# Kernel tuning notes

Hardware: AMD Instinct MI355X
Metric: run time of the kernel (lower is better)

## Reference

```python
import jax, jax.numpy as jnp
import numpy as np

N_QUBITS = 12
N_QLAYERS = 2
BATCH = 1024
DIM = 2 ** N_QUBITS


def _apply_1q(state, U, wire):
    # state: (B, 2**n) complex; U: (2,2) shared or (B,2,2) batched
    B = state.shape[0]
    s = state.reshape(B, 2 ** wire, 2, -1)
    if U.ndim == 2:
        s = jnp.einsum('ij,bajc->baic', U, s)
    else:
        s = jnp.einsum('bij,bajc->baic', U, s)
    return s.reshape(B, DIM)


def _apply_cnot(state, c, t):
    # CNOT with control c, target t on flat state (B, 2**n)
    B = state.shape[0]
    a, b = min(c, t), max(c, t)
    s = state.reshape(B, 2 ** a, 2, 2 ** (b - a - 1), 2, -1)
    ctrl_ax, tgt_ax = (2, 4) if c < t else (4, 2)
    s0 = jnp.take(s, 0, axis=ctrl_ax)
    s1 = jnp.take(s, 1, axis=ctrl_ax)
    flip_ax = tgt_ax - 1 if tgt_ax > ctrl_ax else tgt_ax
    s1 = jnp.flip(s1, axis=flip_ax)  # X on target where control==1
    return jnp.stack([s0, s1], axis=ctrl_ax).reshape(B, DIM)


def _ry_batched(theta):
    # theta: (B,) -> (B,2,2) RY(theta) matrices
    c = jnp.cos(theta * 0.5)
    s = jnp.sin(theta * 0.5)
    U = jnp.stack([jnp.stack([c, -s], -1), jnp.stack([s, c], -1)], -2)
    return U.astype(jnp.complex64)


def _rot(phi, theta, omega):
    # PennyLane Rot = RZ(omega) @ RY(theta) @ RZ(phi)
    c = jnp.cos(theta * 0.5)
    s = jnp.sin(theta * 0.5)
    em = jnp.exp(-0.5j * (phi + omega))   # e^{-i(phi+omega)/2}
    ep = jnp.exp(0.5j * (phi + omega))
    ed = jnp.exp(0.5j * (phi - omega))    # e^{ i(phi-omega)/2}
    edm = jnp.exp(-0.5j * (phi - omega))
    row0 = jnp.stack([em * c, -ed * s])
    row1 = jnp.stack([edm * s, ep * c])
    return jnp.stack([row0, row1]).astype(jnp.complex64)


def _circuit(x, weights):
    B = x.shape[0]
    state = jnp.zeros((B, DIM), jnp.complex64).at[:, 0].set(1.0)
    for l in range(N_QLAYERS):
        # AngleEmbedding: RY(x[:, q]) on each wire (data re-uploading)
        for q in range(N_QUBITS):
            state = _apply_1q(state, _ry_batched(x[:, q]), q)
        # StronglyEntanglingLayers (single layer slice): Rot per wire
        for q in range(N_QUBITS):
            w = weights[l, q]
            state = _apply_1q(state, _rot(w[0], w[1], w[2]), q)
        # range-1 CNOT ring (single-layer SEL => r = 1)
        for q in range(N_QUBITS):
            state = _apply_cnot(state, q, (q + 1) % N_QUBITS)
    probs = state.real ** 2 + state.imag ** 2  # (B, 2**n)
    outs = []
    for q in range(N_QUBITS):
        p = probs.reshape(B, 2 ** q, 2, -1)
        outs.append(jnp.sum(p[:, :, 0, :], axis=(1, 2)) - jnp.sum(p[:, :, 1, :], axis=(1, 2)))
    return jnp.stack(outs, axis=1)  # (B, n_qubits) <Z_q> expvals


def setup_inputs() -> dict:
    key = jax.random.key(0)
    k1, k2 = jax.random.split(key)
    x = jax.random.uniform(k1, (BATCH, N_QUBITS), jnp.float32, 0.0, 2.0 * np.pi)
    weights = jax.random.normal(k2, (N_QLAYERS, N_QUBITS, 3), jnp.float32)
    return {"x": x, "weights": weights}


def reference(x, weights):
    return _circuit(x, weights)
```

## Files before the change

kernel.cpp:

```cpp
#include <hip/hip_runtime.h>

#define NQ 12
#define NT 64
#define EPB 4


struct cpx { float x, y; };
__device__ __forceinline__ cpx cmul(cpx a, cpx b) {
    return { a.x * b.x - a.y * b.y, a.x * b.y + a.y * b.x };
}
__device__ __forceinline__ cpx cmulc(cpx a, cpx b) {
    return { a.x * b.x + a.y * b.y, a.y * b.x - a.x * b.y };
}
__device__ __forceinline__ cpx cadd(cpx a, cpx b) { return { a.x + b.x, a.y + b.y }; }
__device__ __forceinline__ cpx csub(cpx a, cpx b) { return { a.x - b.x, a.y - b.y }; }
__device__ __forceinline__ cpx shflc(cpx a, int lane) {
    cpx r; r.x = __shfl(a.x, lane, 64); r.y = __shfl(a.y, lane, 64); return r;
}

__global__ __launch_bounds__(NT) void qsim_kernel(
    const float* __restrict__ x,
    const float* __restrict__ w,
    float* __restrict__ out)
{
    __shared__ float fm[EPB][2][NQ][8];
    __shared__ cpx Amat[EPB][9][16], Bmat[EPB][9][16];
    __shared__ cpx gS[EPB][4][4];
    __shared__ cpx h0U[EPB][4], h0S[EPB][4], h11U[EPB][4], h11S[EPB][4];
    __shared__ cpx Rv[EPB][3][4][4];
    __shared__ cpx PBc[EPB][11][16];
    __shared__ cpx SAc[EPB][12][16];
    __shared__ float sval[EPB][48];

    const int t    = threadIdx.x;
    const int g    = t >> 4;
    const int u    = t & 15;
    const int base = t & 48;
    const int b0   = blockIdx.x * EPB;

    for (int task = t; task < EPB * 2 * NQ; task += NT) {
        int e = task / (2 * NQ);
        int rem = task % (2 * NQ);
        int l = rem / NQ, q = rem % NQ;
        float hy = 0.5f * x[(b0 + e) * NQ + q];
        float cy = cosf(hy), sy = sinf(hy);
        const float* wp = w + (l * NQ + q) * 3;
        float phi = wp[0], the = wp[1], om = wp[2];
        float c = cosf(0.5f * the), s = sinf(0.5f * the);
        float al = 0.5f * (phi + om), be = 0.5f * (phi - om);
        float ca = cosf(al), sa = sinf(al), cb = cosf(be), sb = sinf(be);
        float r00r =  ca * c, r00i = -sa * c;
        float r01r = -cb * s, r01i = -sb * s;
        float r10r =  cb * s, r10i = -sb * s;
        float r11r =  ca * c, r11i =  sa * c;
        float* m = fm[e][l][q];
        m[0] =  r00r * cy + r01r * sy;  m[1] =  r00i * cy + r01i * sy;
        m[2] = -r00r * sy + r01r * cy;  m[3] = -r00i * sy + r01i * cy;
        m[4] =  r10r * cy + r11r * sy;  m[5] =  r10i * cy + r11i * sy;
        m[6] = -r10r * sy + r11r * cy;  m[7] = -r10i * sy + r11i * cy;
    }
    __syncthreads();

    auto Vq = [&](int q, int bit) -> cpx {
        const float* m = &fm[g][0][q][bit ? 4 : 0]; return { m[0], m[1] };
    };
    auto Uq = [&](int q, int d, int c) -> cpx {
        const float* m = &fm[g][1][q][4 * d + 2 * c]; return { m[0], m[1] };
    };

    {
        const int a = (u >> 3) & 1, ap = (u >> 2) & 1, c = (u >> 1) & 1, cp = u & 1;
        for (int q = 2; q <= 10; ++q) {
            cpx t0 = cmul(Vq(q, c ^ a),  Uq(q, 0, c));
            cpx t1 = cmul(Vq(q, c ^ a),  Uq(q, 1, c));
            cpx p0 = cmul(Vq(q, cp ^ ap), Uq(q, 0, cp));
            cpx p1 = cmul(Vq(q, cp ^ ap), Uq(q, 1, cp));
            cpx e0 = cmulc(t0, p0), e1 = cmulc(t1, p1);
            Amat[g][q - 2][u] = cadd(e0, e1);
            Bmat[g][q - 2][u] = csub(e0, e1);
        }
        const int s = a, sp = ap, cc = c, ccp = cp;
        cpx l0 = cmul(Uq(1, 0, cc),  Vq(1, cc ^ s));
        cpx l1 = cmul(Uq(1, 1, cc),  Vq(1, cc ^ s));
        cpx m0 = cmul(Uq(1, 0, ccp), Vq(1, ccp ^ sp));
        cpx m1 = cmul(Uq(1, 1, ccp), Vq(1, ccp ^ sp));
        cpx gg = csub(cmulc(l0, m0), cmulc(l1, m1));
        cpx lw = cmulc(Vq(0, s), Vq(0, sp));
        gS[g][2 * s + sp][2 * cc + ccp] = cmul(gg, lw);
    }
    if (u < 4) {
        const int c0 = u >> 1, c0p = u & 1;
        cpx a0 = cmulc(Uq(0, 0, c0),  Uq(0, 0, c0p));
        cpx a1 = cmulc(Uq(0, 1, c0),  Uq(0, 1, c0p));
        h0U[g][u] = cadd(a0, a1);  h0S[g][u] = csub(a0, a1);
        cpx b0v = cmulc(Uq(11, 0, c0),  Uq(11, 0, c0p));
        cpx b1v = cmulc(Uq(11, 1, c0),  Uq(11, 1, c0p));
        h11U[g][u] = cadd(b0v, b1v);  h11S[g][u] = csub(b0v, b1v);
    }
    __syncthreads();

    {
        const int s = (u >> 3) & 1, sp = (u >> 2) & 1, c10 = (u >> 1) & 1, c10p = u & 1;
        for (int V = 0; V < 3; ++V) {
            const cpx* h0  = (V == 1) ? h0U[g]  : h0S[g];
            const cpx* h11 = (V == 0) ? h11U[g] : h11S[g];
            cpx acc = { 0.f, 0.f };
            for (int c0 = 0; c0 < 2; ++c0)
                for (int c0p = 0; c0p < 2; ++c0p) {
                    cpx term = cmul(h0[2 * c0 + c0p], h11[2 * (c0 ^ s) + (c0p ^ sp)]);
                    term = cmul(term, Vq(11, c0 ^ s ^ c10));
                    term = cmulc(term, Vq(11, c0p ^ sp ^ c10p));
                    acc = cadd(acc, term);
                }
            Rv[g][V][2 * s + sp][2 * c10 + c10p] = acc;
        }
    }
    __syncthreads();

    {
        const int R = u >> 2, C = u & 3;
        cpx cur = { (R == C) ? 1.f : 0.f, 0.f };
        PBc[g][1][u] = cur;
        for (int k = 2; k <= 10; ++k) {
            cpx nv = { 0.f, 0.f };
            for (int K = 0; K < 4; ++K)
                nv = cadd(nv, cmul(shflc(cur, base + 4 * R + K), Bmat[g][k - 2][4 * K + C]));
            cur = nv;
            PBc[g][k][u] = cur;
        }
        cur = { (R == C) ? 1.f : 0.f, 0.f };
        SAc[g][11][u] = cur;
        for (int k = 10; k >= 2; --k) {
            cpx nv = { 0.f, 0.f };
            for (int K = 0; K < 4; ++K)
                nv = cadd(nv, cmul(Amat[g][k - 2][4 * R + K], shflc(cur, base + 4 * K + C)));
            cur = nv;
            SAc[g][k][u] = cur;
        }
    }
    __syncthreads();

    for (int pi = u; pi < 48; pi += 16) {
        const int qq = pi >> 2, ssi = pi & 3;
        const int kk = (qq == 0 || qq == 11) ? 10 : qq;
        const int V  = (qq == 0) ? 1 : ((qq == 11) ? 2 : 0);
        cpx rowL[4], colR[4];
        for (int K = 0; K < 4; ++K) {
            cpx acc = { 0.f, 0.f };
            for (int R = 0; R < 4; ++R)
                acc = cadd(acc, cmul(gS[g][ssi][R], PBc[g][kk][4 * R + K]));
            rowL[K] = acc;
            cpx acc2 = { 0.f, 0.f };
            for (int C = 0; C < 4; ++C)
                acc2 = cadd(acc2, cmul(SAc[g][kk + 1][4 * K + C], Rv[g][V][ssi][C]));
            colR[K] = acc2;
        }
        cpx val = { 0.f, 0.f };
        for (int K = 0; K < 4; ++K) val = cadd(val, cmul(rowL[K], colR[K]));
        sval[g][pi] = val.x;
    }
    __syncthreads();

    if (t < EPB * NQ) {
        int e = t / NQ, q = t % NQ;
        out[(b0 + e) * NQ + q] =
            sval[e][4 * q] + sval[e][4 * q + 1] + sval[e][4 * q + 2] + sval[e][4 * q + 3];
    }
}

extern "C" void kernel_launch(void* const* d_in, const int* in_sizes, int n_in,
                              void* d_out, int out_size, void* d_ws, size_t ws_size,
                              hipStream_t stream) {
    int xi = 0, wi = 1;
    if (n_in >= 2 && in_sizes[1] > in_sizes[0]) { xi = 1; wi = 0; }
    const float* x = (const float*)d_in[xi];
    const float* w = (const float*)d_in[wi];
    float* out = (float*)d_out;
    const int B = in_sizes[xi] / NQ;
    qsim_kernel<<<B / EPB, NT, 0, stream>>>(x, w, out);
}
```

Baseline: 60.20 us.

## Process one batch element per block and split per-element stages across thread groups

Each block now handles a single batch element with 64 threads instead of four elements with 16 threads each. Within a block the gate-matrix construction, the forward and backward transfer-matrix chains, and the boundary terms are spread across the thread groups so they run concurrently. One barrier is removed, and the final reduction uses wave shuffles instead of shared memory. Trig calls switch to fast intrinsics, which may reduce accuracy. The grid grows fourfold, and several phases leave many lanes idle.

Measured after the change: 58.08 us. 3.5% less time.

```diff
diff --git a/kernel.cpp b/kernel.cpp
--- a/kernel.cpp
+++ b/kernel.cpp
@@ -2,7 +2,6 @@
 
 #define NQ 12
 #define NT 64
-#define EPB 4
 
 
 struct cpx { float x, y; };
@@ -23,37 +22,34 @@
     const float* __restrict__ w,
     float* __restrict__ out)
 {
-    __shared__ float fm[EPB][2][NQ][8];
-    __shared__ cpx Amat[EPB][9][16], Bmat[EPB][9][16];
-    __shared__ cpx gS[EPB][4][4];
-    __shared__ cpx h0U[EPB][4], h0S[EPB][4], h11U[EPB][4], h11S[EPB][4];
-    __shared__ cpx Rv[EPB][3][4][4];
-    __shared__ cpx PBc[EPB][11][16];
-    __shared__ cpx SAc[EPB][12][16];
-    __shared__ float sval[EPB][48];
+    __shared__ float fm[2][NQ][8];
+    __shared__ cpx Amat[9][16], Bmat[9][16];
+    __shared__ cpx gS[4][4];
+    __shared__ cpx h0U[4], h0S[4], h11U[4], h11S[4];
+    __shared__ cpx Rv[3][4][4];
+    __shared__ cpx PBc[11][16];
+    __shared__ cpx SAc[12][16];
 
-    const int t    = threadIdx.x;
-    const int g    = t >> 4;
-    const int u    = t & 15;
-    const int base = t & 48;
-    const int b0   = blockIdx.x * EPB;
+    const int t   = threadIdx.x;
+    const int u   = t & 15;
+    const int grp = t >> 4;
+    const int b   = blockIdx.x;
 
-    for (int task = t; task < EPB * 2 * NQ; task += NT) {
-        int e = task / (2 * NQ);
-        int rem = task % (2 * NQ);
-        int l = rem / NQ, q = rem % NQ;
-        float hy = 0.5f * x[(b0 + e) * NQ + q];
-        float cy = cosf(hy), sy = sinf(hy);
+    if (t < 2 * NQ) {
+        const int l = (t >= NQ) ? 1 : 0;
+        const int q = t - l * NQ;
+        float hy = 0.5f * x[b * NQ + q];
+        float cy = __cosf(hy), sy = __sinf(hy);
         const float* wp = w + (l * NQ + q) * 3;
         float phi = wp[0], the = wp[1], om = wp[2];
-        float c = cosf(0.5f * the), s = sinf(0.5f * the);
+        float cth = __cosf(0.5f * the), sth = __sinf(0.5f * the);
         float al = 0.5f * (phi + om), be = 0.5f * (phi - om);
-        float ca = cosf(al), sa = sinf(al), cb = cosf(be), sb = sinf(be);
-        float r00r =  ca * c, r00i = -sa * c;
-        float r01r = -cb * s, r01i = -sb * s;
-        float r10r =  cb * s, r10i = -sb * s;
-        float r11r =  ca * c, r11i =  sa * c;
-        float* m = fm[e][l][q];
+        float ca = __cosf(al), sa = __sinf(al), cb = __cosf(be), sb = __sinf(be);
+        float r00r =  ca * cth, r00i = -sa * cth;
+        float r01r = -cb * sth, r01i = -sb * sth;
+        float r10r =  cb * sth, r10i = -sb * sth;
+        float r11r =  ca * cth, r11i =  sa * cth;
+        float* m = fm[l][q];
         m[0] =  r00r * cy + r01r * sy;  m[1] =  r00i * cy + r01i * sy;
         m[2] = -r00r * sy + r01r * cy;  m[3] = -r00i * sy + r01i * cy;
         m[4] =  r10r * cy + r11r * sy;  m[5] =  r10i * cy + r11i * sy;
@@ -62,23 +58,26 @@
     __syncthreads();
 
     auto Vq = [&](int q, int bit) -> cpx {
-        const float* m = &fm[g][0][q][bit ? 4 : 0]; return { m[0], m[1] };
+        const float* m = &fm[0][q][bit ? 4 : 0]; return { m[0], m[1] };
     };
     auto Uq = [&](int q, int d, int c) -> cpx {
-        const float* m = &fm[g][1][q][4 * d + 2 * c]; return { m[0], m[1] };
+        const float* m = &fm[1][q][4 * d + 2 * c]; return { m[0], m[1] };
     };
 
-    {
-        const int a = (u >> 3) & 1, ap = (u >> 2) & 1, c = (u >> 1) & 1, cp = u & 1;
-        for (int q = 2; q <= 10; ++q) {
+    const int a = (u >> 3) & 1, ap = (u >> 2) & 1, c = (u >> 1) & 1, cp = u & 1;
+    if (grp < 3) {
+        #pragma unroll
+        for (int r = 0; r < 3; ++r) {
+            const int q = 2 + 3 * grp + r;
             cpx t0 = cmul(Vq(q, c ^ a),  Uq(q, 0, c));
             cpx t1 = cmul(Vq(q, c ^ a),  Uq(q, 1, c));
             cpx p0 = cmul(Vq(q, cp ^ ap), Uq(q, 0, cp));
             cpx p1 = cmul(Vq(q, cp ^ ap), Uq(q, 1, cp));
             cpx e0 = cmulc(t0, p0), e1 = cmulc(t1, p1);
-            Amat[g][q - 2][u] = cadd(e0, e1);
-            Bmat[g][q - 2][u] = csub(e0, e1);
+            Amat[q - 2][u] = cadd(e0, e1);
+            Bmat[q - 2][u] = csub(e0, e1);
         }
+    } else {
         const int s = a, sp = ap, cc = c, ccp = cp;
         cpx l0 = cmul(Uq(1, 0, cc),  Vq(1, cc ^ s));
         cpx l1 = cmul(Uq(1, 1, cc),  Vq(1, cc ^ s));
@@ -86,85 +85,88 @@
         cpx m1 = cmul(Uq(1, 1, ccp), Vq(1, ccp ^ sp));
         cpx gg = csub(cmulc(l0, m0), cmulc(l1, m1));
         cpx lw = cmulc(Vq(0, s), Vq(0, sp));
-        gS[g][2 * s + sp][2 * cc + ccp] = cmul(gg, lw);
-    }
-    if (u < 4) {
-        const int c0 = u >> 1, c0p = u & 1;
-        cpx a0 = cmulc(Uq(0, 0, c0),  Uq(0, 0, c0p));
-        cpx a1 = cmulc(Uq(0, 1, c0),  Uq(0, 1, c0p));
-        h0U[g][u] = cadd(a0, a1);  h0S[g][u] = csub(a0, a1);
-        cpx b0v = cmulc(Uq(11, 0, c0),  Uq(11, 0, c0p));
-        cpx b1v = cmulc(Uq(11, 1, c0),  Uq(11, 1, c0p));
-        h11U[g][u] = cadd(b0v, b1v);  h11S[g][u] = csub(b0v, b1v);
+        gS[2 * s + sp][2 * cc + ccp] = cmul(gg, lw);
+        if (u < 4) {
+            const int c0 = u >> 1, c0p = u & 1;
+            cpx a0 = cmulc(Uq(0, 0, c0),  Uq(0, 0, c0p));
+            cpx a1 = cmulc(Uq(0, 1, c0),  Uq(0, 1, c0p));
+            h0U[u] = cadd(a0, a1);  h0S[u] = csub(a0, a1);
+            cpx b0v = cmulc(Uq(11, 0, c0),  Uq(11, 0, c0p));
+            cpx b1v = cmulc(Uq(11, 1, c0),  Uq(11, 1, c0p));
+            h11U[u] = cadd(b0v, b1v);  h11S[u] = csub(b0v, b1v);
+        }
     }
     __syncthreads();
 
-    {
-        const int s = (u >> 3) & 1, sp = (u >> 2) & 1, c10 = (u >> 1) & 1, c10p = u & 1;
-        for (int V = 0; V < 3; ++V) {
-            const cpx* h0  = (V == 1) ? h0U[g]  : h0S[g];
-            const cpx* h11 = (V == 0) ? h11U[g] : h11S[g];
+    if (t < 32) {
+        const int R = u >> 2, C = u & 3;
+        const bool isA = (t >= 16);
+        const int base = t & 48;
+        cpx rhs[9][4];
+        #pragma unroll
+        for (int i = 0; i < 9; ++i)
+            #pragma unroll
+            for (int K = 0; K < 4; ++K)
+                rhs[i][K] = isA ? Amat[8 - i][4 * C + K] : Bmat[i][4 * K + C];
+        cpx cur = { (R == C) ? 1.f : 0.f, 0.f };
+        { cpx* dst = isA ? &SAc[11][4 * C + R] : &PBc[1][u]; *dst = cur; }
+        #pragma unroll
+        for (int i = 0; i < 9; ++i) {
+            cpx nv = { 0.f, 0.f };
+            #pragma unroll
+            for (int K = 0; K < 4; ++K)
+                nv = cadd(nv, cmul(shflc(cur, base + 4 * R + K), rhs[i][K]));
+            cur = nv;
+            cpx* dst = isA ? &SAc[10 - i][4 * C + R] : &PBc[2 + i][u];
+            *dst = cur;
+        }
+    } else {
+        for (int task = t - 32; task < 48; task += 32) {
+            const int V = task >> 4, uu = task & 15;
+            const int s = (uu >> 3) & 1, sp = (uu >> 2) & 1;
+            const int c10 = (uu >> 1) & 1, c10p = uu & 1;
+            const cpx* h0  = (V == 1) ? h0U  : h0S;
+            const cpx* h11 = (V == 0) ? h11U : h11S;
             cpx acc = { 0.f, 0.f };
+            #pragma unroll
             for (int c0 = 0; c0 < 2; ++c0)
+                #pragma unroll
                 for (int c0p = 0; c0p < 2; ++c0p) {
                     cpx term = cmul(h0[2 * c0 + c0p], h11[2 * (c0 ^ s) + (c0p ^ sp)]);
                     term = cmul(term, Vq(11, c0 ^ s ^ c10));
                     term = cmulc(term, Vq(11, c0p ^ sp ^ c10p));
                     acc = cadd(acc, term);
                 }
-            Rv[g][V][2 * s + sp][2 * c10 + c10p] = acc;
+            Rv[V][2 * s + sp][2 * c10 + c10p] = acc;
         }
     }
     __syncthreads();
 
-    {
-        const int R = u >> 2, C = u & 3;
-        cpx cur = { (R == C) ? 1.f : 0.f, 0.f };
-        PBc[g][1][u] = cur;
-        for (int k = 2; k <= 10; ++k) {
-            cpx nv = { 0.f, 0.f };
-            for (int K = 0; K < 4; ++K)
-                nv = cadd(nv, cmul(shflc(cur, base + 4 * R + K), Bmat[g][k - 2][4 * K + C]));
-            cur = nv;
-            PBc[g][k][u] = cur;
-        }
-        cur = { (R == C) ? 1.f : 0.f, 0.f };
-        SAc[g][11][u] = cur;
-        for (int k = 10; k >= 2; --k) {
-            cpx nv = { 0.f, 0.f };
-            for (int K = 0; K < 4; ++K)
-                nv = cadd(nv, cmul(Amat[g][k - 2][4 * R + K], shflc(cur, base + 4 * K + C)));
-            cur = nv;
-            SAc[g][k][u] = cur;
-        }
-    }
-    __syncthreads();
-
-    for (int pi = u; pi < 48; pi += 16) {
-        const int qq = pi >> 2, ssi = pi & 3;
+    if (t < 48) {
+        const int qq = t >> 2, ssi = t & 3;
         const int kk = (qq == 0 || qq == 11) ? 10 : qq;
         const int V  = (qq == 0) ? 1 : ((qq == 11) ? 2 : 0);
         cpx rowL[4], colR[4];
+        #pragma unroll
         for (int K = 0; K < 4; ++K) {
             cpx acc = { 0.f, 0.f };
+            #pragma unroll
             for (int R = 0; R < 4; ++R)
-                acc = cadd(acc, cmul(gS[g][ssi][R], PBc[g][kk][4 * R + K]));
+                acc = cadd(acc, cmul(gS[ssi][R], PBc[kk][4 * R + K]));
             rowL[K] = acc;
             cpx acc2 = { 0.f, 0.f };
+            #pragma unroll
             for (int C = 0; C < 4; ++C)
-                acc2 = cadd(acc2, cmul(SAc[g][kk + 1][4 * K + C], Rv[g][V][ssi][C]));
+                acc2 = cadd(acc2, cmul(SAc[kk + 1][4 * K + C], Rv[V][ssi][C]));
             colR[K] = acc2;
         }
         cpx val = { 0.f, 0.f };
+        #pragma unroll
         for (int K = 0; K < 4; ++K) val = cadd(val, cmul(rowL[K], colR[K]));
-        sval[g][pi] = val.x;
-    }
-    __syncthreads();
-
-    if (t < EPB * NQ) {
-        int e = t / NQ, q = t % NQ;
-        out[(b0 + e) * NQ + q] =
-            sval[e][4 * q] + sval[e][4 * q + 1] + sval[e][4 * q + 2] + sval[e][4 * q + 3];
+        float vr = val.x;
+        vr += __shfl_xor(vr, 1, 64);
+        vr += __shfl_xor(vr, 2, 64);
+        if ((t & 3) == 0) out[b * NQ + (t >> 2)] = vr;
     }
 }
 
@@ -177,5 +179,5 @@
     const float* w = (const float*)d_in[wi];
     float* out = (float*)d_out;
     const int B = in_sizes[xi] / NQ;
-    qsim_kernel<<<B / EPB, NT, 0, stream>>>(x, w, out);
+    qsim_kernel<<<B, NT, 0, stream>>>(x, w, out);
 }
```
